# Kernel optimization log

Measured on AMD Instinct MI355X. Metric: run time of the kernel, lower is better.

The kernel has to match this reference:

```python
import jax, jax.numpy as jnp
import numpy as np

B, S, H = 4, 2048, 768
NUM_HEADS = 12
HEAD_DIM = H // NUM_HEADS


def setup_inputs() -> dict:
    key = jax.random.key(0)
    k1, k2, k3 = jax.random.split(key, 3)
    hidden_states = jax.random.normal(k1, (B, S, H), dtype=jnp.float32)
    # torch Linear weight [out,in]; store transposed [in,out] for x @ W
    w_qkv = jax.random.normal(k2, (H, 3 * H), dtype=jnp.float32) * (1.0 / np.sqrt(H))
    w_out = jax.random.normal(k3, (H, H), dtype=jnp.float32) * (1.0 / np.sqrt(H))
    return {"hidden_states": hidden_states, "w_qkv": w_qkv, "w_out": w_out}


def reference(hidden_states, w_qkv, w_out):
    b, s, h = hidden_states.shape
    qkv = hidden_states @ w_qkv                      # [b,s,3h]
    qkv = qkv.reshape(b, s, 3, NUM_HEADS, HEAD_DIM)
    qkv = jnp.transpose(qkv, (2, 0, 3, 1, 4))        # [3,b,nh,s,hd]
    q, k, v = qkv[0], qkv[1], qkv[2]
    scale = 1.0 / np.sqrt(HEAD_DIM).astype(np.float32)
    scores = jnp.einsum('bhqd,bhkd->bhqk', q, k) * scale   # [b,nh,s,s]
    causal = jnp.triu(jnp.ones((s, s), dtype=bool), k=1)
    scores = jnp.where(causal, jnp.float32(-jnp.inf), scores)
    attn = jax.nn.softmax(scores, axis=-1)
    # dropout is identity in eval mode
    out = jnp.einsum('bhqk,bhkd->bhqd', attn, v)      # [b,nh,s,hd]
    out = jnp.transpose(out, (0, 2, 1, 3)).reshape(b, s, h)
    return out @ w_out
```

## Files before the change

### kernel.cpp

```cpp
#include <hip/hip_runtime.h>
#include <stdint.h>

#define B_ 4
#define S_ 2048
#define H_ 768
#define NH_ 12
#define HD_ 64
#define BH_ (B_ * NH_)

#define QSCALE 0.18033688011112042f

typedef __attribute__((ext_vector_type(4))) float f32x4;
typedef __attribute__((ext_vector_type(8))) __bf16 bf16x8;
typedef __attribute__((ext_vector_type(8))) unsigned short ushort8;
typedef __attribute__((ext_vector_type(4))) unsigned short ushort4v;

__device__ __forceinline__ unsigned short bf16rne(float f) {
  union { float f; unsigned int u; } v;
  v.f = f;
  unsigned int u = v.u;
  return (unsigned short)((u + 0x7fffu + ((u >> 16) & 1u)) >> 16);
}

#if __has_builtin(__builtin_amdgcn_cvt_pk_bf16_f32)
__device__ __forceinline__ unsigned int pk2(float a, float b) {
  auto r = __builtin_amdgcn_cvt_pk_bf16_f32(a, b);
  return *(unsigned int*)&r;
}
#else
__device__ __forceinline__ unsigned int pk2(float a, float b) {
  return (unsigned int)bf16rne(a) | ((unsigned int)bf16rne(b) << 16);
}
#endif

#if __has_builtin(__builtin_amdgcn_exp2f)
#define EXP2F(x) __builtin_amdgcn_exp2f(x)
#else
#define EXP2F(x) exp2f(x)
#endif

__device__ __forceinline__ void gll16(const void* g, void* l) {
  __builtin_amdgcn_global_load_lds(
      (const __attribute__((address_space(1))) unsigned int*)g,
      (__attribute__((address_space(3))) unsigned int*)l, 16, 0, 0);
}

__device__ __forceinline__ void tconv_body(const float* __restrict__ in,
                                           unsigned short* __restrict__ out,
                                           int R, int C, int bx, int by,
                                           unsigned short (*tile)[72], int tid) {
  int c0 = bx * 64, r0 = by * 64;
#pragma unroll
  for (int i = 0; i < 4; ++i) {
    int c = i * 256 + tid;
    int row = c >> 4, col4 = (c & 15) * 4;
    float4 v = *(const float4*)(in + (size_t)(r0 + row) * C + c0 + col4);
    *(uint2*)(&tile[row][col4]) = (uint2){pk2(v.x, v.y), pk2(v.z, v.w)};
  }
  __syncthreads();
#pragma unroll
  for (int i = 0; i < 2; ++i) {
    int c = i * 256 + tid;
    int oc = c >> 3, r8 = (c & 7) * 8;
    ushort8 v;
#pragma unroll
    for (int j = 0; j < 8; ++j) v[j] = tile[r8 + j][oc];
    *(ushort8*)(out + (size_t)(c0 + oc) * R + r0 + r8) = v;
  }
}

__global__ __launch_bounds__(256) void prep_kernel(const float* __restrict__ hs,
                                                   const float* __restrict__ wqkv,
                                                   const float* __restrict__ wout,
                                                   unsigned short* __restrict__ Xbf,
                                                   unsigned short* __restrict__ Wqkvt,
                                                   unsigned short* __restrict__ Woutt) {
  __shared__ unsigned short tile[64][72];
  int bid = blockIdx.x, tid = threadIdx.x;
  if (bid < 3072) {
    int i = (bid * 256 + tid) * 8;
    const float4* p = (const float4*)(hs + i);
    float4 a = p[0], b = p[1];
    uint4 r = {pk2(a.x, a.y), pk2(a.z, a.w), pk2(b.x, b.y), pk2(b.z, b.w)};
    *(uint4*)(Xbf + i) = r;
  } else if (bid < 3504) {
    int idx = bid - 3072;
    tconv_body(wqkv, Wqkvt, 768, 2304, idx % 36, idx / 36, tile, tid);
  } else {
    int idx = bid - 3504;
    tconv_body(wout, Woutt, 768, 768, idx % 12, idx / 12, tile, tid);
  }
}

template <int MODE>
__device__ __forceinline__ void gemm_core(const unsigned short* __restrict__ A,
                                          const unsigned short* __restrict__ Bm,
                                          void* __restrict__ Cout, int N, int K,
                                          int bm, int bn,
                                          unsigned short* As, unsigned short* Bs) {
  int tid = threadIdx.x;
  int lane = tid & 63, wave = tid >> 6;
  int quad = lane >> 4, l16 = lane & 15;
  int wm = (wave & 1) * 64, wn = (wave >> 1) * 64;
  const unsigned short* Ag = A + (size_t)bm * 128 * K;
  const unsigned short* Bg = Bm + (size_t)bn * 128 * K;

  f32x4 zero = {0.f, 0.f, 0.f, 0.f};
  f32x4 acc[4][4];
#pragma unroll
  for (int mt = 0; mt < 4; ++mt)
#pragma unroll
    for (int nt = 0; nt < 4; ++nt) acc[mt][nt] = zero;

  for (int k0 = 0; k0 < K; k0 += 32) {
#pragma unroll
    for (int i = 0; i < 2; ++i) {
      int c = i * 256 + tid;
      int row = c >> 2, off = (c & 3) * 8;
      gll16(Ag + (size_t)row * K + k0 + off, As + c * 8);
      gll16(Bg + (size_t)row * K + k0 + off, Bs + c * 8);
    }
    __syncthreads();
    bf16x8 af[4], bf[4];
#pragma unroll
    for (int mt = 0; mt < 4; ++mt)
      af[mt] = *(const bf16x8*)(As + (wm + mt * 16 + l16) * 32 + quad * 8);
#pragma unroll
    for (int nt = 0; nt < 4; ++nt)
      bf[nt] = *(const bf16x8*)(Bs + (wn + nt * 16 + l16) * 32 + quad * 8);
#pragma unroll
    for (int mt = 0; mt < 4; ++mt)
#pragma unroll
      for (int nt = 0; nt < 4; ++nt) {
        if (MODE == 2)
          acc[mt][nt] = __builtin_amdgcn_mfma_f32_16x16x32_bf16(af[mt], bf[nt], acc[mt][nt], 0, 0, 0);
        else
          acc[mt][nt] = __builtin_amdgcn_mfma_f32_16x16x32_bf16(bf[nt], af[mt], acc[mt][nt], 0, 0, 0);
      }
    __syncthreads();
  }

  if (MODE == 0) {
    unsigned short* qkv = (unsigned short*)Cout;
    int which = (bn >= 6);
#pragma unroll
    for (int mt = 0; mt < 4; ++mt)
#pragma unroll
      for (int nt = 0; nt < 4; ++nt) {
        int f0 = bn * 128 + wn + nt * 16 + quad * 4;
        int tm = bm * 128 + wm + mt * 16 + l16;
        int rem = f0 - which * 768;
        int head = rem >> 6, d0 = rem & 63;
        int b = tm >> 11, s = tm & 2047;
        if (which == 0) {
          uint2 pkv = {pk2(acc[mt][nt][0] * QSCALE, acc[mt][nt][1] * QSCALE),
                       pk2(acc[mt][nt][2] * QSCALE, acc[mt][nt][3] * QSCALE)};
          *(uint2*)(qkv + (((size_t)b * NH_ + head) * S_ + s) * HD_ + d0) = pkv;
        } else {
          uint2 pkv = {pk2(acc[mt][nt][0], acc[mt][nt][1]),
                       pk2(acc[mt][nt][2], acc[mt][nt][3])};
          int dd0 = (((d0 >> 3) ^ (s & 7)) << 3) | (d0 & 7);
          *(uint2*)(qkv + (((size_t)(BH_ + b * NH_ + head)) * S_ + s) * HD_ + dd0) = pkv;
        }
      }
  } else if (MODE == 2) {
    unsigned short* vt = (unsigned short*)Cout;
#pragma unroll
    for (int mt = 0; mt < 4; ++mt)
#pragma unroll
      for (int nt = 0; nt < 4; ++nt) {
        int f = bn * 128 + wn + nt * 16 + l16;
        int t0 = bm * 128 + wm + mt * 16 + quad * 4;
        int rem = f - 1536;
        int head = rem >> 6, d = rem & 63;
        int b = t0 >> 11, s0 = t0 & 2047;
        int tile = s0 >> 6, sin = s0 & 63;
        int pos = (((sin >> 3) ^ (d & 7)) << 3) | (sin & 7);
        uint2 pkv = {pk2(acc[mt][nt][0], acc[mt][nt][1]),
                     pk2(acc[mt][nt][2], acc[mt][nt][3])};
        *(uint2*)(vt + (((size_t)(b * NH_ + head)) * HD_ + d) * S_ + tile * 64 + pos) = pkv;
      }
  } else {
    float* outp = (float*)Cout;
#pragma unroll
    for (int mt = 0; mt < 4; ++mt)
#pragma unroll
      for (int nt = 0; nt < 4; ++nt) {
        int f0 = bn * 128 + wn + nt * 16 + quad * 4;
        int tm = bm * 128 + wm + mt * 16 + l16;
        *(f32x4*)(outp + (size_t)tm * N + f0) = acc[mt][nt];
      }
  }
}

__global__ __launch_bounds__(256) void gemm_qkv(const unsigned short* __restrict__ A,
                                                const unsigned short* __restrict__ Bm,
                                                unsigned short* __restrict__ QK,
                                                unsigned short* __restrict__ Vt) {
  __shared__ unsigned short As[128 * 32];
  __shared__ unsigned short Bs[128 * 32];
  int bm = blockIdx.x, bn = blockIdx.y;
  if (bn < 12)
    gemm_core<0>(A, Bm, QK, 2304, 768, bm, bn, As, Bs);
  else
    gemm_core<2>(A, Bm, Vt, 2304, 768, bm, bn, As, Bs);
}

__global__ __launch_bounds__(256) void gemm_out(const unsigned short* __restrict__ A,
                                                const unsigned short* __restrict__ Bm,
                                                float* __restrict__ Cout) {
  __shared__ unsigned short As[128 * 32];
  __shared__ unsigned short Bs[128 * 32];
  gemm_core<1>(A, Bm, Cout, 768, 768, blockIdx.x, blockIdx.y, As, Bs);
}

__global__ __launch_bounds__(512, 6) void attn_kernel(const unsigned short* __restrict__ Q,
                                                      const unsigned short* __restrict__ Kg,
                                                      const unsigned short* __restrict__ Vt,
                                                      unsigned short* __restrict__ O) {
  __shared__ unsigned short Ks[2][64 * 64];
  __shared__ unsigned short Vs[2][64 * 64];
  __shared__ unsigned short Ps[8][16 * 64];
  int bh = blockIdx.x;
  int y = blockIdx.y;
  int qt = (y & 1) ? (15 - (y >> 1)) : (y >> 1);
  int tid = threadIdx.x, lane = tid & 63, wave = tid >> 6;
  int quad = lane >> 4, l16 = lane & 15;
  const unsigned short* Qp = Q + (size_t)bh * S_ * HD_;
  const unsigned short* Kp = Kg + (size_t)bh * S_ * HD_;
  const unsigned short* Vp = Vt + (size_t)bh * HD_ * S_;
  int q0 = qt * 128;
  int qrow = q0 + wave * 16 + l16;
  int kmax_w = (q0 + wave * 16 + 15) >> 6;
  int kmax_b = 2 * qt + 1;

  auto stage = [&](int t, int buf) {
    int row = tid >> 3, off = (tid & 7) * 8;
    gll16(Kp + (size_t)t * 64 * HD_ + row * HD_ + off, &Ks[buf][tid * 8]);
    gll16(Vp + (size_t)row * S_ + t * 64 + off, &Vs[buf][tid * 8]);
  };

  stage(0, 0);

  bf16x8 qf[2];
#pragma unroll
  for (int ks = 0; ks < 2; ++ks)
    qf[ks] = *(const bf16x8*)(Qp + (size_t)qrow * HD_ + ks * 32 + quad * 8);

  bf16x8 ones;
#pragma unroll
  for (int j = 0; j < 8; ++j) ones[j] = (__bf16)1.0f;

  f32x4 zero = {0.f, 0.f, 0.f, 0.f};
  float m_i = -1e30f, l_i = 0.f;
  f32x4 o[4];
#pragma unroll
  for (int nt = 0; nt < 4; ++nt) o[nt] = zero;

  for (int t = 0; t <= kmax_b; ++t) {
    __syncthreads();
    if (t < kmax_b) stage(t + 1, (t + 1) & 1);
    if (t > kmax_w) continue;
    const unsigned short* Kb = Ks[t & 1];
    const unsigned short* Vb = Vs[t & 1];

    f32x4 sf[4];
#pragma unroll
    for (int nt = 0; nt < 4; ++nt) sf[nt] = zero;
#pragma unroll
    for (int ks = 0; ks < 2; ++ks)
#pragma unroll
      for (int nt = 0; nt < 4; ++nt) {
        bf16x8 kf = *(const bf16x8*)(Kb + (nt * 16 + l16) * 64 + (((ks * 4 + quad) ^ (l16 & 7)) << 3));
        sf[nt] = __builtin_amdgcn_mfma_f32_16x16x32_bf16(kf, qf[ks], sf[nt], 0, 0, 0);
      }

    if (t == kmax_w) {
#pragma unroll
      for (int nt = 0; nt < 4; ++nt)
#pragma unroll
        for (int r = 0; r < 4; ++r)
          if (t * 64 + nt * 16 + quad * 4 + r > qrow) sf[nt][r] = -1e30f;
    }

    float mx = fmaxf(fmaxf(fmaxf(sf[0][0], sf[0][1]), fmaxf(sf[0][2], sf[0][3])),
                     fmaxf(fmaxf(sf[1][0], sf[1][1]), fmaxf(sf[1][2], sf[1][3])));
    mx = fmaxf(mx, fmaxf(fmaxf(fmaxf(sf[2][0], sf[2][1]), fmaxf(sf[2][2], sf[2][3])),
                         fmaxf(fmaxf(sf[3][0], sf[3][1]), fmaxf(sf[3][2], sf[3][3]))));
    mx = fmaxf(mx, __shfl_xor(mx, 16));
    mx = fmaxf(mx, __shfl_xor(mx, 32));
    float mn = fmaxf(m_i, mx);
    float alpha = EXP2F(m_i - mn);
    m_i = mn;

#pragma unroll
    for (int nt = 0; nt < 4; ++nt) {
      uint2 pkv = {pk2(EXP2F(sf[nt][0] - mn), EXP2F(sf[nt][1] - mn)),
                   pk2(EXP2F(sf[nt][2] - mn), EXP2F(sf[nt][3] - mn))};
      int kvblk = nt * 2 + (quad >> 1);
      *(uint2*)(&Ps[wave][l16 * 64 + (((kvblk ^ (l16 & 7)) << 3) | ((quad & 1) * 4))]) = pkv;
    }

#pragma unroll
    for (int nt = 0; nt < 4; ++nt)
#pragma unroll
      for (int r = 0; r < 4; ++r) o[nt][r] *= alpha;

    f32x4 rsv = zero;
#pragma unroll
    for (int ks = 0; ks < 2; ++ks) {
      bf16x8 pf = *(const bf16x8*)(&Ps[wave][l16 * 64 + (((ks * 4 + quad) ^ (l16 & 7)) << 3)]);
      rsv = __builtin_amdgcn_mfma_f32_16x16x32_bf16(ones, pf, rsv, 0, 0, 0);
#pragma unroll
      for (int nt = 0; nt < 4; ++nt) {
        bf16x8 vf = *(const bf16x8*)(Vb + (nt * 16 + l16) * 64 + (((ks * 4 + quad) ^ (l16 & 7)) << 3));
        o[nt] = __builtin_amdgcn_mfma_f32_16x16x32_bf16(vf, pf, o[nt], 0, 0, 0);
      }
    }
    l_i = l_i * alpha + rsv[0];
  }

  float inv = 1.f / l_i;
  int b = bh / NH_, h = bh % NH_;
#pragma unroll
  for (int nt = 0; nt < 4; ++nt) {
    uint2 pkv = {pk2(o[nt][0] * inv, o[nt][1] * inv),
                 pk2(o[nt][2] * inv, o[nt][3] * inv)};
    int d0 = nt * 16 + quad * 4;
    *(uint2*)(O + ((size_t)b * S_ + qrow) * H_ + h * HD_ + d0) = pkv;
  }
}

extern "C" void kernel_launch(void* const* d_in, const int* in_sizes, int n_in,
                              void* d_out, int out_size, void* d_ws, size_t ws_size,
                              hipStream_t stream) {
  (void)in_sizes; (void)n_in; (void)out_size; (void)ws_size;
  const float* hs = (const float*)d_in[0];
  const float* wqkv = (const float*)d_in[1];
  const float* wout = (const float*)d_in[2];
  float* out = (float*)d_out;

  unsigned short* Xbf = (unsigned short*)d_ws;
  unsigned short* Wqkvt = Xbf + (size_t)8192 * 768;
  unsigned short* Woutt = Wqkvt + (size_t)2304 * 768;
  unsigned short* QK = Woutt + (size_t)768 * 768;
  unsigned short* Vt = QK + (size_t)2 * BH_ * S_ * HD_;
  unsigned short* Attn = Xbf;

  prep_kernel<<<3648, 256, 0, stream>>>(hs, wqkv, wout, Xbf, Wqkvt, Woutt);
  gemm_qkv<<<dim3(64, 18), 256, 0, stream>>>(Xbf, Wqkvt, QK, Vt);
  attn_kernel<<<dim3(48, 16), 512, 0, stream>>>(QK, QK + (size_t)BH_ * S_ * HD_, Vt, Attn);
  gemm_out<<<dim3(64, 6), 256, 0, stream>>>(Attn, Woutt, out);
}
```

Baseline: 207.0 us.

## Switch GEMM core to 32x32x16 MFMA with swizzled LDS and rebalance attention tile order

The shared GEMM core now uses 32x32x16 bf16 MFMA instructions with 2x2 f32x16 accumulators per wave instead of 4x4 16x16x32 tiles. It also XOR-swizzles the 16-byte column blocks in LDS to reduce bank conflicts on fragment reads. The epilogues are rewritten for the 32x32 output layout. Separately, the attention kernel maps each block to a query tile through a permutation offset by batch-head, to spread causal work more evenly across CUs.

```diff
diff --git a/kernel.cpp b/kernel.cpp
--- a/kernel.cpp
+++ b/kernel.cpp
@@ -11,9 +11,9 @@
 #define QSCALE 0.18033688011112042f
 
 typedef __attribute__((ext_vector_type(4))) float f32x4;
+typedef __attribute__((ext_vector_type(16))) float f32x16;
 typedef __attribute__((ext_vector_type(8))) __bf16 bf16x8;
 typedef __attribute__((ext_vector_type(8))) unsigned short ushort8;
-typedef __attribute__((ext_vector_type(4))) unsigned short ushort4v;
 
 __device__ __forceinline__ unsigned short bf16rne(float f) {
   union { float f; unsigned int u; } v;
@@ -100,43 +100,53 @@
                                           unsigned short* As, unsigned short* Bs) {
   int tid = threadIdx.x;
   int lane = tid & 63, wave = tid >> 6;
-  int quad = lane >> 4, l16 = lane & 15;
+  int l32 = lane & 31, lh = lane >> 5;
   int wm = (wave & 1) * 64, wn = (wave >> 1) * 64;
   const unsigned short* Ag = A + (size_t)bm * 128 * K;
   const unsigned short* Bg = Bm + (size_t)bn * 128 * K;
 
-  f32x4 zero = {0.f, 0.f, 0.f, 0.f};
-  f32x4 acc[4][4];
-#pragma unroll
-  for (int mt = 0; mt < 4; ++mt)
-#pragma unroll
-    for (int nt = 0; nt < 4; ++nt) acc[mt][nt] = zero;
+  f32x16 acc[2][2];
+#pragma unroll
+  for (int mb = 0; mb < 2; ++mb)
+#pragma unroll
+    for (int nb = 0; nb < 2; ++nb)
+#pragma unroll
+      for (int e = 0; e < 16; ++e) acc[mb][nb][e] = 0.f;
 
   for (int k0 = 0; k0 < K; k0 += 32) {
 #pragma unroll
     for (int i = 0; i < 2; ++i) {
       int c = i * 256 + tid;
-      int row = c >> 2, off = (c & 3) * 8;
+      int row = c >> 2, blk = c & 3;
+      int off = ((blk ^ (row & 3)) * 8);
       gll16(Ag + (size_t)row * K + k0 + off, As + c * 8);
       gll16(Bg + (size_t)row * K + k0 + off, Bs + c * 8);
     }
     __syncthreads();
-    bf16x8 af[4], bf[4];
-#pragma unroll
-    for (int mt = 0; mt < 4; ++mt)
-      af[mt] = *(const bf16x8*)(As + (wm + mt * 16 + l16) * 32 + quad * 8);
-#pragma unroll
-    for (int nt = 0; nt < 4; ++nt)
-      bf[nt] = *(const bf16x8*)(Bs + (wn + nt * 16 + l16) * 32 + quad * 8);
-#pragma unroll
-    for (int mt = 0; mt < 4; ++mt)
-#pragma unroll
-      for (int nt = 0; nt < 4; ++nt) {
-        if (MODE == 2)
-          acc[mt][nt] = __builtin_amdgcn_mfma_f32_16x16x32_bf16(af[mt], bf[nt], acc[mt][nt], 0, 0, 0);
-        else
-          acc[mt][nt] = __builtin_amdgcn_mfma_f32_16x16x32_bf16(bf[nt], af[mt], acc[mt][nt], 0, 0, 0);
-      }
+#pragma unroll
+    for (int kh = 0; kh < 2; ++kh) {
+      int j = kh * 2 + lh;
+      bf16x8 af[2], bf[2];
+#pragma unroll
+      for (int mb = 0; mb < 2; ++mb) {
+        int row = wm + mb * 32 + l32;
+        af[mb] = *(const bf16x8*)(As + row * 32 + ((j ^ (row & 3)) * 8));
+      }
+#pragma unroll
+      for (int nb = 0; nb < 2; ++nb) {
+        int row = wn + nb * 32 + l32;
+        bf[nb] = *(const bf16x8*)(Bs + row * 32 + ((j ^ (row & 3)) * 8));
+      }
+#pragma unroll
+      for (int mb = 0; mb < 2; ++mb)
+#pragma unroll
+        for (int nb = 0; nb < 2; ++nb) {
+          if (MODE == 2)
+            acc[mb][nb] = __builtin_amdgcn_mfma_f32_32x32x16_bf16(af[mb], bf[nb], acc[mb][nb], 0, 0, 0);
+          else
+            acc[mb][nb] = __builtin_amdgcn_mfma_f32_32x32x16_bf16(bf[nb], af[mb], acc[mb][nb], 0, 0, 0);
+        }
+    }
     __syncthreads();
   }
 
@@ -144,51 +154,62 @@
     unsigned short* qkv = (unsigned short*)Cout;
     int which = (bn >= 6);
 #pragma unroll
-    for (int mt = 0; mt < 4; ++mt)
-#pragma unroll
-      for (int nt = 0; nt < 4; ++nt) {
-        int f0 = bn * 128 + wn + nt * 16 + quad * 4;
-        int tm = bm * 128 + wm + mt * 16 + l16;
-        int rem = f0 - which * 768;
-        int head = rem >> 6, d0 = rem & 63;
+    for (int mb = 0; mb < 2; ++mb)
+#pragma unroll
+      for (int nb = 0; nb < 2; ++nb) {
+        int tm = bm * 128 + wm + mb * 32 + l32;
         int b = tm >> 11, s = tm & 2047;
-        if (which == 0) {
-          uint2 pkv = {pk2(acc[mt][nt][0] * QSCALE, acc[mt][nt][1] * QSCALE),
-                       pk2(acc[mt][nt][2] * QSCALE, acc[mt][nt][3] * QSCALE)};
-          *(uint2*)(qkv + (((size_t)b * NH_ + head) * S_ + s) * HD_ + d0) = pkv;
-        } else {
-          uint2 pkv = {pk2(acc[mt][nt][0], acc[mt][nt][1]),
-                       pk2(acc[mt][nt][2], acc[mt][nt][3])};
-          int dd0 = (((d0 >> 3) ^ (s & 7)) << 3) | (d0 & 7);
-          *(uint2*)(qkv + (((size_t)(BH_ + b * NH_ + head)) * S_ + s) * HD_ + dd0) = pkv;
+#pragma unroll
+        for (int g = 0; g < 4; ++g) {
+          int f0 = bn * 128 + wn + nb * 32 + g * 8 + lh * 4;
+          int rem = f0 - which * 768;
+          int head = rem >> 6, d0 = rem & 63;
+          if (which == 0) {
+            uint2 pkv = {pk2(acc[mb][nb][g * 4 + 0] * QSCALE, acc[mb][nb][g * 4 + 1] * QSCALE),
+                         pk2(acc[mb][nb][g * 4 + 2] * QSCALE, acc[mb][nb][g * 4 + 3] * QSCALE)};
+            *(uint2*)(qkv + (((size_t)b * NH_ + head) * S_ + s) * HD_ + d0) = pkv;
+          } else {
+            uint2 pkv = {pk2(acc[mb][nb][g * 4 + 0], acc[mb][nb][g * 4 + 1]),
+                         pk2(acc[mb][nb][g * 4 + 2], acc[mb][nb][g * 4 + 3])};
+            int dd0 = (((d0 >> 3) ^ (s & 7)) << 3) | (d0 & 7);
+            *(uint2*)(qkv + (((size_t)(BH_ + b * NH_ + head)) * S_ + s) * HD_ + dd0) = pkv;
+          }
         }
       }
   } else if (MODE == 2) {
     unsigned short* vt = (unsigned short*)Cout;
 #pragma unroll
-    for (int mt = 0; mt < 4; ++mt)
-#pragma unroll
-      for (int nt = 0; nt < 4; ++nt) {
-        int f = bn * 128 + wn + nt * 16 + l16;
-        int t0 = bm * 128 + wm + mt * 16 + quad * 4;
+    for (int mb = 0; mb < 2; ++mb)
+#pragma unroll
+      for (int nb = 0; nb < 2; ++nb) {
+        int f = bn * 128 + wn + nb * 32 + l32;
         int rem = f - 1536;
         int head = rem >> 6, d = rem & 63;
-        int b = t0 >> 11, s0 = t0 & 2047;
-        int tile = s0 >> 6, sin = s0 & 63;
-        int pos = (((sin >> 3) ^ (d & 7)) << 3) | (sin & 7);
-        uint2 pkv = {pk2(acc[mt][nt][0], acc[mt][nt][1]),
-                     pk2(acc[mt][nt][2], acc[mt][nt][3])};
-        *(uint2*)(vt + (((size_t)(b * NH_ + head)) * HD_ + d) * S_ + tile * 64 + pos) = pkv;
+#pragma unroll
+        for (int g = 0; g < 4; ++g) {
+          int t0 = bm * 128 + wm + mb * 32 + g * 8 + lh * 4;
+          int b = t0 >> 11, s0 = t0 & 2047;
+          int tile = s0 >> 6, sin = s0 & 63;
+          int pos = (((sin >> 3) ^ (d & 7)) << 3) | (sin & 7);
+          uint2 pkv = {pk2(acc[mb][nb][g * 4 + 0], acc[mb][nb][g * 4 + 1]),
+                       pk2(acc[mb][nb][g * 4 + 2], acc[mb][nb][g * 4 + 3])};
+          *(uint2*)(vt + (((size_t)(b * NH_ + head)) * HD_ + d) * S_ + tile * 64 + pos) = pkv;
+        }
       }
   } else {
     float* outp = (float*)Cout;
 #pragma unroll
-    for (int mt = 0; mt < 4; ++mt)
-#pragma unroll
-      for (int nt = 0; nt < 4; ++nt) {
-        int f0 = bn * 128 + wn + nt * 16 + quad * 4;
-        int tm = bm * 128 + wm + mt * 16 + l16;
-        *(f32x4*)(outp + (size_t)tm * N + f0) = acc[mt][nt];
+    for (int mb = 0; mb < 2; ++mb)
+#pragma unroll
+      for (int nb = 0; nb < 2; ++nb) {
+        int tm = bm * 128 + wm + mb * 32 + l32;
+#pragma unroll
+        for (int g = 0; g < 4; ++g) {
+          int f0 = bn * 128 + wn + nb * 32 + g * 8 + lh * 4;
+          f32x4 v = {acc[mb][nb][g * 4 + 0], acc[mb][nb][g * 4 + 1],
+                     acc[mb][nb][g * 4 + 2], acc[mb][nb][g * 4 + 3]};
+          *(f32x4*)(outp + (size_t)tm * N + f0) = v;
+        }
       }
   }
 }
@@ -221,9 +242,10 @@
   __shared__ unsigned short Ks[2][64 * 64];
   __shared__ unsigned short Vs[2][64 * 64];
   __shared__ unsigned short Ps[8][16 * 64];
+  const int pi_[16] = {0, 1, 3, 5, 7, 9, 11, 13, 15, 14, 12, 10, 8, 6, 4, 2};
   int bh = blockIdx.x;
   int y = blockIdx.y;
-  int qt = (y & 1) ? (15 - (y >> 1)) : (y >> 1);
+  int qt = pi_[(bh + y) & 15];
   int tid = threadIdx.x, lane = tid & 63, wave = tid >> 6;
   int quad = lane >> 4, l16 = lane & 15;
   const unsigned short* Qp = Q + (size_t)bh * S_ * HD_;
```

New measurement: 214.2 us. +3.4%, slower.

## Double-buffer GEMM LDS tiles, swap grid order, remap attention tile schedule

Applied to the files above, without the earlier changes.

The QKV and output GEMMs now use double-buffered shared-memory tiles. The next K-slice is issued before the current one is consumed, and the trailing barrier per iteration is dropped. This is meant to overlap global loads with MFMA work. The grid axes are swapped so consecutive blocks walk along N and share the same A rows in cache. The attention kernel replaces its interleaved query-tile order with a permutation indexed by (bh+y), to spread causal work more evenly across concurrently scheduled blocks. Doubling the LDS use per GEMM block can lower occupancy.

```diff
diff --git a/kernel.cpp b/kernel.cpp
--- a/kernel.cpp
+++ b/kernel.cpp
@@ -13,7 +13,6 @@
 typedef __attribute__((ext_vector_type(4))) float f32x4;
 typedef __attribute__((ext_vector_type(8))) __bf16 bf16x8;
 typedef __attribute__((ext_vector_type(8))) unsigned short ushort8;
-typedef __attribute__((ext_vector_type(4))) unsigned short ushort4v;
 
 __device__ __forceinline__ unsigned short bf16rne(float f) {
   union { float f; unsigned int u; } v;
@@ -105,29 +104,37 @@
   const unsigned short* Ag = A + (size_t)bm * 128 * K;
   const unsigned short* Bg = Bm + (size_t)bn * 128 * K;
 
-  f32x4 zero = {0.f, 0.f, 0.f, 0.f};
-  f32x4 acc[4][4];
-#pragma unroll
-  for (int mt = 0; mt < 4; ++mt)
-#pragma unroll
-    for (int nt = 0; nt < 4; ++nt) acc[mt][nt] = zero;
-
-  for (int k0 = 0; k0 < K; k0 += 32) {
+  auto stage = [&](int k, int buf) {
 #pragma unroll
     for (int i = 0; i < 2; ++i) {
       int c = i * 256 + tid;
       int row = c >> 2, off = (c & 3) * 8;
-      gll16(Ag + (size_t)row * K + k0 + off, As + c * 8);
-      gll16(Bg + (size_t)row * K + k0 + off, Bs + c * 8);
+      gll16(Ag + (size_t)row * K + k * 32 + off, As + buf * 4096 + c * 8);
+      gll16(Bg + (size_t)row * K + k * 32 + off, Bs + buf * 4096 + c * 8);
     }
+  };
+
+  f32x4 zero = {0.f, 0.f, 0.f, 0.f};
+  f32x4 acc[4][4];
+#pragma unroll
+  for (int mt = 0; mt < 4; ++mt)
+#pragma unroll
+    for (int nt = 0; nt < 4; ++nt) acc[mt][nt] = zero;
+
+  const int NK = K / 32;
+  stage(0, 0);
+  for (int k = 0; k < NK; ++k) {
     __syncthreads();
+    if (k + 1 < NK) stage(k + 1, (k + 1) & 1);
+    const unsigned short* Ab = As + (k & 1) * 4096;
+    const unsigned short* Bb = Bs + (k & 1) * 4096;
     bf16x8 af[4], bf[4];
 #pragma unroll
     for (int mt = 0; mt < 4; ++mt)
-      af[mt] = *(const bf16x8*)(As + (wm + mt * 16 + l16) * 32 + quad * 8);
+      af[mt] = *(const bf16x8*)(Ab + (wm + mt * 16 + l16) * 32 + quad * 8);
 #pragma unroll
     for (int nt = 0; nt < 4; ++nt)
-      bf[nt] = *(const bf16x8*)(Bs + (wn + nt * 16 + l16) * 32 + quad * 8);
+      bf[nt] = *(const bf16x8*)(Bb + (wn + nt * 16 + l16) * 32 + quad * 8);
 #pragma unroll
     for (int mt = 0; mt < 4; ++mt)
 #pragma unroll
@@ -137,7 +144,6 @@
         else
           acc[mt][nt] = __builtin_amdgcn_mfma_f32_16x16x32_bf16(bf[nt], af[mt], acc[mt][nt], 0, 0, 0);
       }
-    __syncthreads();
   }
 
   if (MODE == 0) {
@@ -197,9 +203,9 @@
                                                 const unsigned short* __restrict__ Bm,
                                                 unsigned short* __restrict__ QK,
                                                 unsigned short* __restrict__ Vt) {
-  __shared__ unsigned short As[128 * 32];
-  __shared__ unsigned short Bs[128 * 32];
-  int bm = blockIdx.x, bn = blockIdx.y;
+  __shared__ unsigned short As[2 * 128 * 32];
+  __shared__ unsigned short Bs[2 * 128 * 32];
+  int bn = blockIdx.x, bm = blockIdx.y;
   if (bn < 12)
     gemm_core<0>(A, Bm, QK, 2304, 768, bm, bn, As, Bs);
   else
@@ -209,9 +215,9 @@
 __global__ __launch_bounds__(256) void gemm_out(const unsigned short* __restrict__ A,
                                                 const unsigned short* __restrict__ Bm,
                                                 float* __restrict__ Cout) {
-  __shared__ unsigned short As[128 * 32];
-  __shared__ unsigned short Bs[128 * 32];
-  gemm_core<1>(A, Bm, Cout, 768, 768, blockIdx.x, blockIdx.y, As, Bs);
+  __shared__ unsigned short As[2 * 128 * 32];
+  __shared__ unsigned short Bs[2 * 128 * 32];
+  gemm_core<1>(A, Bm, Cout, 768, 768, blockIdx.y, blockIdx.x, As, Bs);
 }
 
 __global__ __launch_bounds__(512, 6) void attn_kernel(const unsigned short* __restrict__ Q,
@@ -221,9 +227,10 @@
   __shared__ unsigned short Ks[2][64 * 64];
   __shared__ unsigned short Vs[2][64 * 64];
   __shared__ unsigned short Ps[8][16 * 64];
+  const int pi_[16] = {0, 1, 3, 5, 7, 9, 11, 13, 15, 14, 12, 10, 8, 6, 4, 2};
   int bh = blockIdx.x;
   int y = blockIdx.y;
-  int qt = (y & 1) ? (15 - (y >> 1)) : (y >> 1);
+  int qt = pi_[(bh + y) & 15];
   int tid = threadIdx.x, lane = tid & 63, wave = tid >> 6;
   int quad = lane >> 4, l16 = lane & 15;
   const unsigned short* Qp = Q + (size_t)bh * S_ * HD_;
@@ -348,7 +355,7 @@
   unsigned short* Attn = Xbf;
 
   prep_kernel<<<3648, 256, 0, stream>>>(hs, wqkv, wout, Xbf, Wqkvt, Woutt);
-  gemm_qkv<<<dim3(64, 18), 256, 0, stream>>>(Xbf, Wqkvt, QK, Vt);
+  gemm_qkv<<<dim3(18, 64), 256, 0, stream>>>(Xbf, Wqkvt, QK, Vt);
   attn_kernel<<<dim3(48, 16), 512, 0, stream>>>(QK, QK + (size_t)BH_ * S_ * HD_, Vt, Attn);
-  gemm_out<<<dim3(64, 6), 256, 0, stream>>>(Attn, Woutt, out);
-}
+  gemm_out<<<dim3(6, 64), 256, 0, stream>>>(Attn, Woutt, out);
+}
```

Measured after the change: 213.9 us. +3.3%, slower.
